# Kernel tuning notes

Hardware: AMD Instinct MI355X
Metric: run time of the kernel (lower is better)

Reference implementation:

```python
import jax, jax.numpy as jnp
import numpy as np

N_ITERS = 5

def setup_inputs() -> dict:
    key = jax.random.key(0)
    k_in, k_ind, k_w = jax.random.split(key, 3)
    inputs = jax.random.normal(k_in, (2, 256, 256, 1), dtype=jnp.float32)
    # indices must be valid for spatial dims [256,256] (iter 1) and [217,721] (iters 2-5)
    ind1 = jax.random.randint(k_ind, (367, 217, 721, 2), 0, 217, dtype=jnp.int32)
    w1 = jax.random.uniform(k_w, (367, 217, 721, 1, 1), dtype=jnp.float32)
    lambda1 = jnp.asarray(0.1, dtype=jnp.float32)
    return {"inputs": inputs, "ind1": ind1, "w1": w1, "lambda1": lambda1}


def reference(inputs, ind1, w1, lambda1):
    # inputs: [B,H,W,C]; ind1: [367,217,721,2]; w1: [367,217,721,1,1]; lambda1: scalar
    i0 = ind1[..., 0]  # [367,217,721] -> indexes dim0 of [H,W,C,B]
    i1 = ind1[..., 1]  # [367,217,721] -> indexes dim1
    y = inputs
    for _ in range(N_ITERS):
        yt = jnp.transpose(y, (1, 2, 3, 0))          # [H,W,C,B]
        gathered = yt[i0, i1]                        # [367,217,721,C,B] (gather_nd)
        y = jnp.sum(gathered * w1, axis=0)           # [217,721,C,B]
        y = jnp.transpose(y, (3, 0, 1, 2))           # [B,217,721,C]
        y = lambda1 * y
    return y
```

## Files before the change

kernel.cpp:

```cpp
#include <hip/hip_runtime.h>
#include <hip/hip_fp16.h>
#include <stdint.h>

#define K_    367
#define P_    217
#define Q_    721
#define QC    217
#define CPQ   (QC*QC)
#define CPQV  47092
#define TPQ   109368
#define YSTR  47104
#define PQ_   (P_*Q_)
#define TOT   ((long long)K_*PQ_)
#define NPAIR (TOT/2)
#define NVC   (CPQV/4)
#define NVT   (TPQ/4)
#define NPAD  (3*K_)
#define LDSH  47092

typedef uint32_t u32x4 __attribute__((ext_vector_type(4)));
typedef float    f32x2 __attribute__((ext_vector_type(2)));

__device__ __forceinline__ uint32_t encode_entry(int i0, int i1, float wv) {
    uint32_t idx2 = ((uint32_t)(i0 * QC + i1)) << 1;
    uint32_t hb = (uint32_t)__half_as_ushort(__float2half(wv));
    return idx2 | (hb << 17);
}
__device__ __forceinline__ void store_entry(uint32_t ui, uint32_t v,
    uint32_t* __restrict__ cornerS, uint32_t* __restrict__ tailS) {
    uint32_t k = ui / (uint32_t)PQ_;
    uint32_t rem = ui - k * (uint32_t)PQ_;
    uint32_t p = rem / (uint32_t)Q_;
    uint32_t q = rem - p * (uint32_t)Q_;
    if (q < QC) cornerS[k * (uint32_t)CPQV + p * QC + q] = v;
    else        tailS[(long long)k * TPQ + p * 504 + (q - QC)] = v;
}

#define GATHER(X, ACC) { uint32_t x_ = (X); \
    float g_ = __half2float(*(const __half*)((const char*)ylds + (x_ & 0x1FFFEu))); \
    float w_ = __half2float(__ushort_as_half((unsigned short)(x_ >> 17))); \
    ACC = fmaf(w_, g_, ACC); }

#define FILL_LDS() { \
    const float4* s4_ = (const float4*)yplane; \
    __half2* d2_ = (__half2*)ylds; \
    for (int i_ = threadIdx.x; i_ < LDSH / 4; i_ += 1024) { \
        float4 v_ = s4_[i_]; \
        d2_[2 * i_]     = __floats2half2_rn(v_.x, v_.y); \
        d2_[2 * i_ + 1] = __floats2half2_rn(v_.z, v_.w); \
    } }

__global__ __launch_bounds__(256) void pack_all(
    const int2* __restrict__ ind, const float* __restrict__ w,
    const float* __restrict__ inp,
    uint32_t* __restrict__ cornerS, uint32_t* __restrict__ tailS,
    float* __restrict__ ybase, float* __restrict__ out)
{
    long long id = (long long)blockIdx.x * 256 + threadIdx.x;
    if (id < NPAIR) {
        long long i = id * 2;
        u32x4 r  = __builtin_nontemporal_load((const u32x4*)(ind + i));
        f32x2 wv = __builtin_nontemporal_load((const f32x2*)(w + i));
        uint32_t v0 = encode_entry((int)r.x, (int)r.y, wv.x);
        uint32_t v1 = encode_entry((int)r.z, (int)r.w, wv.y);
        store_entry((uint32_t)i,      v0, cornerS, tailS);
        store_entry((uint32_t)i + 1u, v1, cornerS, tailS);
        return;
    }
    if (id == NPAIR) {
        long long i = TOT - 1;
        int2 e = ind[i];
        store_entry((uint32_t)i, encode_entry(e.x, e.y, w[i]), cornerS, tailS);
        return;
    }
    long long e = id - (NPAIR + 1);
    if (e < CPQ) {
        int o = (int)e;
        int p = o / QC, q = o - p * QC;
        ybase[o]        = inp[p * 256 + q];
        ybase[YSTR + o] = inp[65536 + p * 256 + q];
        return;
    }
    e -= CPQ;
    if (e < NPAD) {
        int k = (int)(e / 3);
        cornerS[(long long)k * CPQV + CPQ + (int)(e - (long long)k * 3)] = 0u;
        return;
    }
    e -= NPAD;
    if (e < 8 * YSTR) {
        ybase[2 * YSTR + e] = 0.f;
        return;
    }
    e -= 8 * YSTR;
    if (e < 2 * PQ_) out[e] = 0.f;
}

__global__ __launch_bounds__(1024) void iter_corner(
    const uint32_t* __restrict__ cs, const float* __restrict__ yin,
    float* __restrict__ yout, const float* __restrict__ lam_p, int KS)
{
    __shared__ __half ylds[LDSH];
    const int bz = blockIdx.z;
    const float* __restrict__ yplane = yin + (size_t)bz * YSTR;
    FILL_LDS();
    __syncthreads();
    const int gx = (NVC + 1023) / 1024;
    const int nunits = gx * KS;
    const float ls = *lam_p;
    const uint4* cs4 = (const uint4*)cs;
    for (int unit = blockIdx.x; unit < nunits; unit += gridDim.x) {
        int ob = unit % gx, kc = unit / gx;
        int ov = ob * 1024 + threadIdx.x;
        if (ov >= NVC) continue;
        int k0 = kc * K_ / KS, k1 = (kc + 1) * K_ / KS;
        float a0 = 0.f, a1 = 0.f, a2 = 0.f, a3 = 0.f;
        const uint4* pp = cs4 + (long long)k0 * NVC + ov;
        #pragma unroll 8
        for (int k = k0; k < k1; ++k, pp += NVC) {
            uint4 v = *pp;
            GATHER(v.x, a0); GATHER(v.y, a1); GATHER(v.z, a2); GATHER(v.w, a3);
        }
        float* op = yout + (size_t)bz * YSTR + 4 * ov;
        atomicAdd(op + 0, a0 * ls);
        atomicAdd(op + 1, a1 * ls);
        atomicAdd(op + 2, a2 * ls);
        atomicAdd(op + 3, a3 * ls);
    }
}

__global__ __launch_bounds__(1024) void iter_final(
    const uint32_t* __restrict__ cs, const uint32_t* __restrict__ ts,
    const float* __restrict__ yin, float* __restrict__ out,
    const float* __restrict__ lam_p, int KS)
{
    __shared__ __half ylds[LDSH];
    const int bz = blockIdx.z;
    const float* __restrict__ yplane = yin + (size_t)bz * YSTR;
    FILL_LDS();
    __syncthreads();
    const int NV = NVC + NVT;
    const int gx = (NV + 1023) / 1024;
    const int nunits = gx * KS;
    const float ls = *lam_p;
    for (int unit = blockIdx.x; unit < nunits; unit += gridDim.x) {
        int ob = unit % gx, kc = unit / gx;
        int ov = ob * 1024 + threadIdx.x;
        if (ov >= NV) continue;
        bool corner = ov < NVC;
        int lv = corner ? ov : ov - NVC;
        int stride = corner ? NVC : NVT;
        const uint4* base = corner ? (const uint4*)cs : (const uint4*)ts;
        int k0 = kc * K_ / KS, k1 = (kc + 1) * K_ / KS;
        float a0 = 0.f, a1 = 0.f, a2 = 0.f, a3 = 0.f;
        const uint4* pp = base + (long long)k0 * stride + lv;
        #pragma unroll 8
        for (int k = k0; k < k1; ++k, pp += stride) {
            uint4 v = *pp;
            GATHER(v.x, a0); GATHER(v.y, a1); GATHER(v.z, a2); GATHER(v.w, a3);
        }
        float acc[4] = {a0, a1, a2, a3};
        int o0 = 4 * lv;
        #pragma unroll
        for (int j = 0; j < 4; ++j) {
            int oo = o0 + j;
            int pos;
            if (corner) {
                if (oo >= CPQ) continue;
                int p = oo / QC; pos = p * Q_ + (oo - p * QC);
            } else {
                int p = oo / 504; pos = p * Q_ + QC + (oo - p * 504);
            }
            atomicAdd(&out[(size_t)bz * PQ_ + pos], acc[j] * ls);
        }
    }
}

extern "C" void kernel_launch(void* const* d_in, const int* in_sizes, int n_in,
                              void* d_out, int out_size, void* d_ws, size_t ws_size,
                              hipStream_t stream)
{
    const float* inp = (const float*)d_in[0];
    const int2*  ind = (const int2*)d_in[1];
    const float* w1  = (const float*)d_in[2];
    const float* lam = (const float*)d_in[3];
    float* out = (float*)d_out;

    size_t cbytes = ((((size_t)K_ * CPQV) * 4) + 255) & ~(size_t)255;
    size_t tbytes = ((((size_t)K_ * TPQ) * 4) + 255) & ~(size_t)255;
    size_t YB = (size_t)(2 * YSTR) * sizeof(float);
    if (ws_size < cbytes + tbytes + 5 * YB) return;

    uint8_t* ws = (uint8_t*)d_ws;
    uint32_t* cornerS = (uint32_t*)ws;
    uint32_t* tailS   = (uint32_t*)(ws + cbytes);
    float* ybase = (float*)(ws + cbytes + tbytes);
    float* y[5];
    for (int i = 0; i < 5; ++i) y[i] = ybase + (size_t)i * (2 * YSTR);

    long long nwork = NPAIR + 1 + CPQ + NPAD + 8LL * YSTR + 2LL * PQ_;
    unsigned nb = (unsigned)((nwork + 255) / 256);
    pack_all<<<dim3(nb), 256, 0, stream>>>(ind, w1, inp, cornerS, tailS, ybase, out);

    dim3 gC(120, 1, 2), gF(117, 1, 2);
    for (int it = 0; it < 4; ++it)
        iter_corner<<<gC, 1024, 0, stream>>>(cornerS, y[it], y[it + 1], lam, 10);
    iter_final<<<gF, 1024, 0, stream>>>(cornerS, tailS, y[4], out, lam, 6);
}
```

Measured before the change: 344.5 us.

## Split packing: pack corner upfront, pack tail inside corner iterations

The pack kernel now encodes only the corner region (q<217) up front. Packing of the tail region is spread across the four corner-iteration kernels, each handling one eighth per batch-plane block set. The aim is to overlap the bandwidth-heavy tail packing with the LDS-gather-bound corner iterations and shorten the serial pack phase. The tail work is tied to the fixed 120-block grid and iteration count, and corner packing now does strided, less coalesced reads of ind and w.

Measured after the change: 399.0 us. 1.16x slower.

```diff
diff --git a/kernel.cpp b/kernel.cpp
--- a/kernel.cpp
+++ b/kernel.cpp
@@ -12,28 +12,18 @@
 #define YSTR  47104
 #define PQ_   (P_*Q_)
 #define TOT   ((long long)K_*PQ_)
-#define NPAIR (TOT/2)
+#define NC    ((long long)K_*CPQ)
+#define NTAIL ((long long)K_*TPQ)
+#define SL    (NTAIL/8)
 #define NVC   (CPQV/4)
 #define NVT   (TPQ/4)
 #define NPAD  (3*K_)
 #define LDSH  47092
 
-typedef uint32_t u32x4 __attribute__((ext_vector_type(4)));
-typedef float    f32x2 __attribute__((ext_vector_type(2)));
-
 __device__ __forceinline__ uint32_t encode_entry(int i0, int i1, float wv) {
     uint32_t idx2 = ((uint32_t)(i0 * QC + i1)) << 1;
     uint32_t hb = (uint32_t)__half_as_ushort(__float2half(wv));
     return idx2 | (hb << 17);
-}
-__device__ __forceinline__ void store_entry(uint32_t ui, uint32_t v,
-    uint32_t* __restrict__ cornerS, uint32_t* __restrict__ tailS) {
-    uint32_t k = ui / (uint32_t)PQ_;
-    uint32_t rem = ui - k * (uint32_t)PQ_;
-    uint32_t p = rem / (uint32_t)Q_;
-    uint32_t q = rem - p * (uint32_t)Q_;
-    if (q < QC) cornerS[k * (uint32_t)CPQV + p * QC + q] = v;
-    else        tailS[(long long)k * TPQ + p * 504 + (q - QC)] = v;
 }
 
 #define GATHER(X, ACC) { uint32_t x_ = (X); \
@@ -50,30 +40,29 @@
         d2_[2 * i_ + 1] = __floats2half2_rn(v_.z, v_.w); \
     } }
 
-__global__ __launch_bounds__(256) void pack_all(
+__global__ __launch_bounds__(256) void pack_corner(
     const int2* __restrict__ ind, const float* __restrict__ w,
     const float* __restrict__ inp,
-    uint32_t* __restrict__ cornerS, uint32_t* __restrict__ tailS,
-    float* __restrict__ ybase, float* __restrict__ out)
+    uint32_t* __restrict__ cornerS, float* __restrict__ ybase,
+    float* __restrict__ out)
 {
     long long id = (long long)blockIdx.x * 256 + threadIdx.x;
-    if (id < NPAIR) {
-        long long i = id * 2;
-        u32x4 r  = __builtin_nontemporal_load((const u32x4*)(ind + i));
-        f32x2 wv = __builtin_nontemporal_load((const f32x2*)(w + i));
-        uint32_t v0 = encode_entry((int)r.x, (int)r.y, wv.x);
-        uint32_t v1 = encode_entry((int)r.z, (int)r.w, wv.y);
-        store_entry((uint32_t)i,      v0, cornerS, tailS);
-        store_entry((uint32_t)i + 1u, v1, cornerS, tailS);
-        return;
-    }
-    if (id == NPAIR) {
-        long long i = TOT - 1;
-        int2 e = ind[i];
-        store_entry((uint32_t)i, encode_entry(e.x, e.y, w[i]), cornerS, tailS);
-        return;
-    }
-    long long e = id - (NPAIR + 1);
+    if (id < NC) {
+        uint32_t o = (uint32_t)id;
+        uint32_t k = o / (uint32_t)CPQ;
+        uint32_t r = o - k * (uint32_t)CPQ;
+        uint32_t p = r / (uint32_t)QC;
+        uint32_t q = r - p * (uint32_t)QC;
+        long long raw = (long long)k * PQ_ + p * Q_ + q;
+        unsigned long long rr =
+            __builtin_nontemporal_load((const unsigned long long*)(ind + raw));
+        float wv = __builtin_nontemporal_load(w + raw);
+        cornerS[k * (uint32_t)CPQV + r] =
+            encode_entry((int)(uint32_t)(rr & 0xFFFFFFFFull),
+                         (int)(uint32_t)(rr >> 32), wv);
+        return;
+    }
+    long long e = id - NC;
     if (e < CPQ) {
         int o = (int)e;
         int p = o / QC, q = o - p * QC;
@@ -96,36 +85,59 @@
     if (e < 2 * PQ_) out[e] = 0.f;
 }
 
-__global__ __launch_bounds__(1024) void iter_corner(
-    const uint32_t* __restrict__ cs, const float* __restrict__ yin,
-    float* __restrict__ yout, const float* __restrict__ lam_p, int KS)
+__global__ __launch_bounds__(1024) void iter_corner_fused(
+    const uint32_t* __restrict__ cs,
+    const int2* __restrict__ ind, const float* __restrict__ w,
+    uint32_t* __restrict__ tailS,
+    const float* __restrict__ yin, float* __restrict__ yout,
+    const float* __restrict__ lam_p, int it)
 {
     __shared__ __half ylds[LDSH];
     const int bz = blockIdx.z;
     const float* __restrict__ yplane = yin + (size_t)bz * YSTR;
     FILL_LDS();
     __syncthreads();
-    const int gx = (NVC + 1023) / 1024;
-    const int nunits = gx * KS;
     const float ls = *lam_p;
+    const int lb = blockIdx.x;
     const uint4* cs4 = (const uint4*)cs;
-    for (int unit = blockIdx.x; unit < nunits; unit += gridDim.x) {
-        int ob = unit % gx, kc = unit / gx;
+
+    {
+        int ob = lb % 12, kc = lb / 12;
+        int k0 = kc * K_ / 10, k1 = (kc + 1) * K_ / 10;
         int ov = ob * 1024 + threadIdx.x;
-        if (ov >= NVC) continue;
-        int k0 = kc * K_ / KS, k1 = (kc + 1) * K_ / KS;
-        float a0 = 0.f, a1 = 0.f, a2 = 0.f, a3 = 0.f;
-        const uint4* pp = cs4 + (long long)k0 * NVC + ov;
-        #pragma unroll 8
-        for (int k = k0; k < k1; ++k, pp += NVC) {
-            uint4 v = *pp;
-            GATHER(v.x, a0); GATHER(v.y, a1); GATHER(v.z, a2); GATHER(v.w, a3);
-        }
-        float* op = yout + (size_t)bz * YSTR + 4 * ov;
-        atomicAdd(op + 0, a0 * ls);
-        atomicAdd(op + 1, a1 * ls);
-        atomicAdd(op + 2, a2 * ls);
-        atomicAdd(op + 3, a3 * ls);
+        if (ov < NVC) {
+            float a0 = 0.f, a1 = 0.f, a2 = 0.f, a3 = 0.f;
+            const uint4* pp = cs4 + (long long)k0 * NVC + ov;
+            #pragma unroll 8
+            for (int k = k0; k < k1; ++k, pp += NVC) {
+                uint4 v = *pp;
+                GATHER(v.x, a0); GATHER(v.y, a1); GATHER(v.z, a2); GATHER(v.w, a3);
+            }
+            float* op = yout + (size_t)bz * YSTR + 4 * ov;
+            atomicAdd(op + 0, a0 * ls);
+            atomicAdd(op + 1, a1 * ls);
+            atomicAdd(op + 2, a2 * ls);
+            atomicAdd(op + 3, a3 * ls);
+        }
+    }
+
+    {
+        long long t0 = (long long)(it * 2 + bz) * SL;
+        long long t1 = t0 + SL;
+        for (long long t = t0 + (long long)lb * 1024 + threadIdx.x; t < t1;
+             t += 120LL * 1024) {
+            uint32_t tt = (uint32_t)t;
+            uint32_t k = tt / (uint32_t)TPQ;
+            uint32_t r = tt - k * (uint32_t)TPQ;
+            uint32_t p = r / 504u;
+            uint32_t q2 = r - p * 504u;
+            long long raw = (long long)k * PQ_ + p * Q_ + QC + q2;
+            unsigned long long rr =
+                __builtin_nontemporal_load((const unsigned long long*)(ind + raw));
+            float wv = __builtin_nontemporal_load(w + raw);
+            tailS[tt] = encode_entry((int)(uint32_t)(rr & 0xFFFFFFFFull),
+                                     (int)(uint32_t)(rr >> 32), wv);
+        }
     }
 }
 
@@ -198,12 +210,13 @@
     float* y[5];
     for (int i = 0; i < 5; ++i) y[i] = ybase + (size_t)i * (2 * YSTR);
 
-    long long nwork = NPAIR + 1 + CPQ + NPAD + 8LL * YSTR + 2LL * PQ_;
+    long long nwork = NC + CPQ + NPAD + 8LL * YSTR + 2LL * PQ_;
     unsigned nb = (unsigned)((nwork + 255) / 256);
-    pack_all<<<dim3(nb), 256, 0, stream>>>(ind, w1, inp, cornerS, tailS, ybase, out);
+    pack_corner<<<dim3(nb), 256, 0, stream>>>(ind, w1, inp, cornerS, ybase, out);
 
     dim3 gC(120, 1, 2), gF(117, 1, 2);
     for (int it = 0; it < 4; ++it)
-        iter_corner<<<gC, 1024, 0, stream>>>(cornerS, y[it], y[it + 1], lam, 10);
+        iter_corner_fused<<<gC, 1024, 0, stream>>>(cornerS, ind, w1, tailS,
+                                                   y[it], y[it + 1], lam, it);
     iter_final<<<gF, 1024, 0, stream>>>(cornerS, tailS, y[4], out, lam, 6);
 }
```
